# Optimization experiments

Measured on AMD Instinct MI355X. Metric: run time of the kernel, lower is better.

Reference implementation:

```python
import jax, jax.numpy as jnp
import numpy as np

K = 3       # conv-transpose kernel size
STRIDE = 2  # conv-transpose stride
PAD = 1     # conv-transpose padding
POOL = 6    # fused pool: MaxPool3d(2,2) then MaxPool3d(3,3) == MaxPool3d(6,6)


def setup_inputs() -> dict:
    key = jax.random.key(0)
    k1, k2, k3 = jax.random.split(key, 3)
    x = jax.random.normal(k1, (8, 16, 32, 32, 32), dtype=jnp.float32)
    weight = jax.random.normal(k2, (16, 32, K, K, K), dtype=jnp.float32)  # [C_in, C_out, k, k, k]
    bias = jax.random.normal(k3, (32,), dtype=jnp.float32)
    return {"x": x, "weight": weight, "bias": bias}


def _conv_transpose3d(x, weight, bias):
    # Transposed conv as dilated conv: lhs_dilation=stride, pad k-1-p, flip kernel.
    # weight layout [C_in, C_out, kd, kh, kw] matches kernel spec 'IODHW'.
    pad = K - 1 - PAD
    y = jax.lax.conv_general_dilated(
        x,
        jnp.flip(weight, axis=(2, 3, 4)),
        window_strides=(1, 1, 1),
        padding=[(pad, pad)] * 3,
        lhs_dilation=(STRIDE, STRIDE, STRIDE),
        dimension_numbers=("NCDHW", "IODHW", "NCDHW"),
    )
    return y + bias[None, :, None, None, None]


def reference(x, weight, bias):
    y = _conv_transpose3d(x, weight, bias)  # [N, C_out, 63, 63, 63]
    n, c, d, h, w = y.shape
    do, ho, wo = d // POOL, h // POOL, w // POOL
    # fused non-overlapping 6x6x6 max pool (== MaxPool3d(2) -> MaxPool3d(3))
    y = y[:, :, : do * POOL, : ho * POOL, : wo * POOL]
    y = y.reshape(n, c, do, POOL, ho, POOL, wo, POOL).max(axis=(3, 5, 7))
    # channel sum, keepdim -> [N, 1, do, ho, wo]
    return jnp.sum(y, axis=1, keepdims=True)
```

## Files before the change

### kernel.cpp

```cpp
#include <hip/hip_runtime.h>
#include <hip/hip_bf16.h>
#include <math.h>


namespace {

typedef __attribute__((ext_vector_type(8))) short short8;
typedef __attribute__((ext_vector_type(16))) float f32x16;

__constant__ int JK[27] = {13, 12, 14, 10, 16, 9,  11, 15, 17, 4,  22, 3,  5, 21,
                           23, 1,  7,  19, 25, 0,  2,  6,  8,  18, 20, 24, 26};

__device__ __forceinline__ uint f2bf(float f) {
  uint u = __float_as_uint(f);
  return (u + 0x7FFFu + ((u >> 16) & 1u)) >> 16;
}

__global__ void prep_w(const float* __restrict__ w, ushort* __restrict__ w2) {
  const int o = blockIdx.x * 256 + threadIdx.x;
  const int t2 = o >> 9;
  const int cih = (o >> 8) & 1;
  const int co = (o >> 3) & 31;
  const int ci = cih * 8 + (o & 7);
  w2[o] = (ushort)f2bf(w[(ci * 32 + co) * 27 + JK[t2]]);
}

template <int PA, int PB, int PC, int BASE>
__device__ __forceinline__ float cls_max(const ushort* __restrict__ w2l,
                                         const char* __restrict__ xw, int lin0,
                                         int lin1, int sz0, int sz1, int hi) {
  constexpr int NTZ = PA ? 2 : 1, NTY = PB ? 2 : 1, NTX = PC ? 2 : 1;
  constexpr int NT = NTZ * NTY * NTX;
  short8 bv[NT];
#pragma unroll
  for (int t = 0; t < NT; ++t)
    bv[t] = *reinterpret_cast<const short8*>(w2l + (BASE + t) * 512);

  f32x16 d;
#pragma unroll
  for (int i = 0; i < 16; ++i) d[i] = 0.f;
#pragma unroll
  for (int a = 0; a < NTZ; ++a) {
    const int oz = PA ? (a ? 0 : 1) : 0;
#pragma unroll
    for (int b = 0; b < NTY; ++b) {
      const int oy = PB ? (b ? 0 : 1) : 0;
#pragma unroll
      for (int c = 0; c < NTX; ++c) {
        const int ox = PC ? (c ? 0 : 1) : 0;
        const int addr =
            ((oz ? lin1 : lin0) + (oy * 4 + ox) * 48) ^ (oz ? sz1 : sz0);
        const short8 av = *reinterpret_cast<const short8*>(xw + addr);
        d = __builtin_amdgcn_mfma_f32_32x32x16_bf16(
            av, bv[(a * NTY + b) * NTX + c], d, 0, 0, 0);
      }
    }
  }
  float ma = d[0];
#pragma unroll
  for (int i = 1; i < 12; ++i) ma = fmaxf(ma, d[i]);
  const float mb = fmaxf(d[12], fmaxf(d[13], d[14]));
  return hi ? ma : fmaxf(ma, mb);
}

__global__ __launch_bounds__(256, 4) void fused_mfma(
    const float* __restrict__ x, const ushort* __restrict__ w2,
    const float* __restrict__ bias, float* __restrict__ out) {
  __shared__ __align__(16) char xls[4 * 3072];

  const int t = threadIdx.x;
  const int wv = t >> 6;
  const int l = t & 63;
  const int hi = l >> 5;
  const int co = l & 31;

  const int cell = blockIdx.x * 4 + wv;
  const int pw = cell % 10;
  const int ph = (cell / 10) % 10;
  const int pd = (cell / 100) % 10;
  const int n = cell / 1000;

  char* xw = xls + wv * 3072;
  {
    const int xi = l & 3, yi = (l >> 2) & 3, zi = l >> 4;
    const float* xg = x + (size_t)n * 524288 + (size_t)(3 * pd + zi) * 1024 +
                      (3 * ph + yi) * 32 + (3 * pw + xi);
    uint pk[8];
#pragma unroll
    for (int q = 0; q < 8; ++q) {
      const uint h0 = f2bf(xg[(2 * q) * 32768]);
      const uint h1 = f2bf(xg[(2 * q + 1) * 32768]);
      pk[q] = (h0 & 0xFFFFu) | (h1 << 16);
    }
    const int swz = (zi & 3) << 4;
    const int a0 = (l * 48) ^ swz;
    const int a1 = (l * 48 + 16) ^ swz;
    *reinterpret_cast<uint4*>(xw + a0) = make_uint4(pk[0], pk[1], pk[2], pk[3]);
    *reinterpret_cast<uint4*>(xw + a1) = make_uint4(pk[4], pk[5], pk[6], pk[7]);
  }
  asm volatile("s_waitcnt lgkmcnt(0)" ::: "memory");

  int p = co > 26 ? 26 : co;
  const int ip = p / 9, jp = (p / 3) % 3, kp = p % 3;
  const int lin0 = (ip * 16 + jp * 4 + kp) * 48 + hi * 16;
  const int lin1 = ((ip + 1) * 16 + jp * 4 + kp) * 48 + hi * 16;
  const int sz0 = (ip & 3) << 4;
  const int sz1 = ((ip + 1) & 3) << 4;

  const ushort* w2l = w2 + hi * 256 + co * 8;

  float cm = cls_max<1, 1, 1, 19>(w2l, xw, lin0, lin1, sz0, sz1, hi);
  cm = fmaxf(cm, cls_max<1, 1, 0, 15>(w2l, xw, lin0, lin1, sz0, sz1, hi));
  cm = fmaxf(cm, cls_max<1, 0, 1, 11>(w2l, xw, lin0, lin1, sz0, sz1, hi));
  cm = fmaxf(cm, cls_max<1, 0, 0, 9>(w2l, xw, lin0, lin1, sz0, sz1, hi));
  cm = fmaxf(cm, cls_max<0, 1, 1, 5>(w2l, xw, lin0, lin1, sz0, sz1, hi));
  cm = fmaxf(cm, cls_max<0, 1, 0, 3>(w2l, xw, lin0, lin1, sz0, sz1, hi));
  cm = fmaxf(cm, cls_max<0, 0, 1, 1>(w2l, xw, lin0, lin1, sz0, sz1, hi));
  cm = fmaxf(cm, cls_max<0, 0, 0, 0>(w2l, xw, lin0, lin1, sz0, sz1, hi));
  cm = fmaxf(cm, __shfl_xor(cm, 32));

  float r = cm + bias[co];
#pragma unroll
  for (int off = 16; off >= 1; off >>= 1) r += __shfl_xor(r, off);
  if (l == 0) out[cell] = r;
}

}

extern "C" void kernel_launch(void* const* d_in, const int* in_sizes, int n_in,
                              void* d_out, int out_size, void* d_ws,
                              size_t ws_size, hipStream_t stream) {
  const float* x = (const float*)d_in[0];
  const float* w = (const float*)d_in[1];
  const float* b = (const float*)d_in[2];
  float* out = (float*)d_out;
  ushort* w2 = (ushort*)d_ws;
  prep_w<<<54, 256, 0, stream>>>(w, w2);
  fused_mfma<<<2000, 256, 0, stream>>>(x, w2, b, out);
}
```

Baseline: 81.96 us.

## Load a whole pooled row per block with coalesced float4 loads and split classes

Each block now handles a full row of 10 pooled cells for one (n, pd, ph) instead of one cell per wave. The shared input slab is loaded cooperatively with float4 reads and written in a swizzled bf16 layout, which replaces the strided scalar gathers and removes the overlap between neighbouring cells. The eight parity classes are split into two halves assigned to different waves, and partial maxima are combined through shared memory after a block barrier. Blocks are also remapped across batch indices. The costs are a block-wide sync, extra shared memory for the reductions, and weights that are no longer preloaded into registers.

```diff
diff --git a/kernel.cpp b/kernel.cpp
--- a/kernel.cpp
+++ b/kernel.cpp
@@ -1,5 +1,4 @@
 #include <hip/hip_runtime.h>
-#include <hip/hip_bf16.h>
 #include <math.h>
 
 
@@ -25,20 +24,24 @@
   w2[o] = (ushort)f2bf(w[(ci * 32 + co) * 27 + JK[t2]]);
 }
 
-template <int PA, int PB, int PC, int BASE>
-__device__ __forceinline__ float cls_max(const ushort* __restrict__ w2l,
-                                         const char* __restrict__ xw, int lin0,
-                                         int lin1, int sz0, int sz1, int hi) {
+struct Pre {
+  uint a[2][2][2];
+};
+
+__device__ __forceinline__ f32x16 zero16() {
+  f32x16 d;
+#pragma unroll
+  for (int i = 0; i < 16; ++i) d[i] = 0.f;
+  return d;
+}
+
+template <int CC, int BASE>
+__device__ __forceinline__ void class_accum(f32x16& d,
+                                            const ushort* __restrict__ w2l,
+                                            const Pre& pre,
+                                            const char* __restrict__ xb) {
+  constexpr int PA = (CC >> 2) & 1, PB = (CC >> 1) & 1, PC = CC & 1;
   constexpr int NTZ = PA ? 2 : 1, NTY = PB ? 2 : 1, NTX = PC ? 2 : 1;
-  constexpr int NT = NTZ * NTY * NTX;
-  short8 bv[NT];
-#pragma unroll
-  for (int t = 0; t < NT; ++t)
-    bv[t] = *reinterpret_cast<const short8*>(w2l + (BASE + t) * 512);
-
-  f32x16 d;
-#pragma unroll
-  for (int i = 0; i < 16; ++i) d[i] = 0.f;
 #pragma unroll
   for (int a = 0; a < NTZ; ++a) {
     const int oz = PA ? (a ? 0 : 1) : 0;
@@ -48,25 +51,73 @@
 #pragma unroll
       for (int c = 0; c < NTX; ++c) {
         const int ox = PC ? (c ? 0 : 1) : 0;
-        const int addr =
-            ((oz ? lin1 : lin0) + (oy * 4 + ox) * 48) ^ (oz ? sz1 : sz0);
-        const short8 av = *reinterpret_cast<const short8*>(xw + addr);
-        d = __builtin_amdgcn_mfma_f32_32x32x16_bf16(
-            av, bv[(a * NTY + b) * NTX + c], d, 0, 0, 0);
+        const short8 bv = *reinterpret_cast<const short8*>(
+            w2l + (BASE + (a * NTY + b) * NTX + c) * 512);
+        const short8 av =
+            *reinterpret_cast<const short8*>(xb + pre.a[oz][oy][ox]);
+        d = __builtin_amdgcn_mfma_f32_32x32x16_bf16(av, bv, d, 0, 0, 0);
       }
     }
   }
+}
+
+__device__ __forceinline__ float rowmax(const f32x16& d, int hi) {
   float ma = d[0];
 #pragma unroll
   for (int i = 1; i < 12; ++i) ma = fmaxf(ma, d[i]);
-  const float mb = fmaxf(d[12], fmaxf(d[13], d[14]));
+  const float mb = fmaxf(fmaxf(d[12], d[13]), d[14]);
   return hi ? ma : fmaxf(ma, mb);
+}
+
+template <int SP>
+__device__ __forceinline__ void do_cell(int pw, int l, int hi, int co, int kp,
+                                        const uint lin[2][2],
+                                        const int zy4[2][2],
+                                        const ushort* __restrict__ w2l,
+                                        const ushort* __restrict__ xs,
+                                        float* __restrict__ red) {
+  Pre pre;
+  const int cellk = 3 * pw + kp;
+#pragma unroll
+  for (int oz = 0; oz < 2; ++oz)
+#pragma unroll
+    for (int oy = 0; oy < 2; ++oy)
+#pragma unroll
+      for (int ox = 0; ox < 2; ++ox) {
+        const int xcol = cellk + ox;
+        pre.a[oz][oy][ox] = (lin[oz][oy] + (uint)(xcol << 5)) ^
+                            ((uint)(((zy4[oz][oy] ^ (xcol >> 2)) & 7)) << 4);
+      }
+  const char* xb = reinterpret_cast<const char*>(xs);
+
+  f32x16 d = zero16();
+  if (SP == 0) class_accum<7, 19>(d, w2l, pre, xb);
+  else         class_accum<6, 15>(d, w2l, pre, xb);
+  float m = rowmax(d, hi);
+  d = zero16();
+  if (SP == 0) class_accum<0, 0>(d, w2l, pre, xb);
+  else         class_accum<1, 1>(d, w2l, pre, xb);
+  m = fmaxf(m, rowmax(d, hi));
+  m = fmaxf(m, __shfl_xor(m, 32));
+  if (l < 32) red[(pw * 4 + (SP == 0 ? 0 : 1)) * 32 + co] = m;
+
+  d = zero16();
+  if (SP == 0) class_accum<5, 11>(d, w2l, pre, xb);
+  else         class_accum<3, 5>(d, w2l, pre, xb);
+  m = rowmax(d, hi);
+  d = zero16();
+  if (SP == 0) class_accum<2, 3>(d, w2l, pre, xb);
+  else         class_accum<4, 9>(d, w2l, pre, xb);
+  m = fmaxf(m, rowmax(d, hi));
+  m = fmaxf(m, __shfl_xor(m, 32));
+  if (l < 32) red[(pw * 4 + (SP == 0 ? 2 : 3)) * 32 + co] = m;
 }
 
 __global__ __launch_bounds__(256, 4) void fused_mfma(
     const float* __restrict__ x, const ushort* __restrict__ w2,
     const float* __restrict__ bias, float* __restrict__ out) {
-  __shared__ __align__(16) char xls[4 * 3072];
+  __shared__ __align__(16) ushort xs[8192];
+  __shared__ float red[10 * 4 * 32];
 
   const int t = threadIdx.x;
   const int wv = t >> 6;
@@ -74,55 +125,67 @@
   const int hi = l >> 5;
   const int co = l & 31;
 
-  const int cell = blockIdx.x * 4 + wv;
-  const int pw = cell % 10;
-  const int ph = (cell / 10) % 10;
-  const int pd = (cell / 100) % 10;
-  const int n = cell / 1000;
-
-  char* xw = xls + wv * 3072;
+  const int lb = (blockIdx.x & 7) * 100 + (blockIdx.x >> 3);
+  const int n = lb / 100, pd = (lb / 10) % 10, ph = lb % 10;
+
   {
-    const int xi = l & 3, yi = (l >> 2) & 3, zi = l >> 4;
-    const float* xg = x + (size_t)n * 524288 + (size_t)(3 * pd + zi) * 1024 +
-                      (3 * ph + yi) * 32 + (3 * pw + xi);
-    uint pk[8];
-#pragma unroll
-    for (int q = 0; q < 8; ++q) {
-      const uint h0 = f2bf(xg[(2 * q) * 32768]);
-      const uint h1 = f2bf(xg[(2 * q + 1) * 32768]);
-      pk[q] = (h0 & 0xFFFFu) | (h1 << 16);
+    const float* xg =
+        x + (size_t)n * 524288 + (size_t)(3 * pd) * 1024 + (3 * ph) * 32;
+#pragma unroll
+    for (int j = 0; j < 8; ++j) {
+      const int fi = j * 256 + t;
+      const int r = fi >> 3;
+      const int xq = fi & 7;
+      const int ci = r >> 4, z = (r >> 2) & 3, y = r & 3;
+      const float4 v = *reinterpret_cast<const float4*>(
+          xg + (size_t)ci * 32768 + z * 1024 + y * 32 + xq * 4);
+      const uint base = (uint)((z << 12) + (y << 10) + ((ci >> 3) << 4) +
+                               ((ci & 7) << 1));
+      const uint swz = (uint)((((z * 4 + y) ^ xq) & 7)) << 4;
+      char* xb = reinterpret_cast<char*>(xs);
+      *(ushort*)(xb + ((base + ((uint)(4 * xq + 0) << 5)) ^ swz)) =
+          (ushort)f2bf(v.x);
+      *(ushort*)(xb + ((base + ((uint)(4 * xq + 1) << 5)) ^ swz)) =
+          (ushort)f2bf(v.y);
+      *(ushort*)(xb + ((base + ((uint)(4 * xq + 2) << 5)) ^ swz)) =
+          (ushort)f2bf(v.z);
+      *(ushort*)(xb + ((base + ((uint)(4 * xq + 3) << 5)) ^ swz)) =
+          (ushort)f2bf(v.w);
     }
-    const int swz = (zi & 3) << 4;
-    const int a0 = (l * 48) ^ swz;
-    const int a1 = (l * 48 + 16) ^ swz;
-    *reinterpret_cast<uint4*>(xw + a0) = make_uint4(pk[0], pk[1], pk[2], pk[3]);
-    *reinterpret_cast<uint4*>(xw + a1) = make_uint4(pk[4], pk[5], pk[6], pk[7]);
   }
-  asm volatile("s_waitcnt lgkmcnt(0)" ::: "memory");
-
-  int p = co > 26 ? 26 : co;
+  __syncthreads();
+
+  const int p = co > 26 ? 26 : co;
   const int ip = p / 9, jp = (p / 3) % 3, kp = p % 3;
-  const int lin0 = (ip * 16 + jp * 4 + kp) * 48 + hi * 16;
-  const int lin1 = ((ip + 1) * 16 + jp * 4 + kp) * 48 + hi * 16;
-  const int sz0 = (ip & 3) << 4;
-  const int sz1 = ((ip + 1) & 3) << 4;
+  uint lin[2][2];
+  int zy4[2][2];
+#pragma unroll
+  for (int oz = 0; oz < 2; ++oz)
+#pragma unroll
+    for (int oy = 0; oy < 2; ++oy) {
+      const int z = ip + oz, y = jp + oy;
+      lin[oz][oy] = (uint)((z << 12) + (y << 10) + (hi << 4));
+      zy4[oz][oy] = z * 4 + y;
+    }
 
   const ushort* w2l = w2 + hi * 256 + co * 8;
 
-  float cm = cls_max<1, 1, 1, 19>(w2l, xw, lin0, lin1, sz0, sz1, hi);
-  cm = fmaxf(cm, cls_max<1, 1, 0, 15>(w2l, xw, lin0, lin1, sz0, sz1, hi));
-  cm = fmaxf(cm, cls_max<1, 0, 1, 11>(w2l, xw, lin0, lin1, sz0, sz1, hi));
-  cm = fmaxf(cm, cls_max<1, 0, 0, 9>(w2l, xw, lin0, lin1, sz0, sz1, hi));
-  cm = fmaxf(cm, cls_max<0, 1, 1, 5>(w2l, xw, lin0, lin1, sz0, sz1, hi));
-  cm = fmaxf(cm, cls_max<0, 1, 0, 3>(w2l, xw, lin0, lin1, sz0, sz1, hi));
-  cm = fmaxf(cm, cls_max<0, 0, 1, 1>(w2l, xw, lin0, lin1, sz0, sz1, hi));
-  cm = fmaxf(cm, cls_max<0, 0, 0, 0>(w2l, xw, lin0, lin1, sz0, sz1, hi));
-  cm = fmaxf(cm, __shfl_xor(cm, 32));
-
-  float r = cm + bias[co];
-#pragma unroll
-  for (int off = 16; off >= 1; off >>= 1) r += __shfl_xor(r, off);
-  if (l == 0) out[cell] = r;
+  for (int c = wv; c < 10; c += 4)
+    do_cell<0>(c, l, hi, co, kp, lin, zy4, w2l, xs, red);
+  for (int c = (wv + 2) & 3; c < 10; c += 4)
+    do_cell<1>(c, l, hi, co, kp, lin, zy4, w2l, xs, red);
+
+  __syncthreads();
+
+  for (int c = wv; c < 10; c += 4) {
+    float v = red[(c * 4 + 0) * 32 + co];
+#pragma unroll
+    for (int s = 1; s < 4; ++s) v = fmaxf(v, red[(c * 4 + s) * 32 + co]);
+    v += bias[co];
+#pragma unroll
+    for (int off = 16; off >= 1; off >>= 1) v += __shfl_xor(v, off);
+    if (l == 0) out[lb * 10 + c] = v;
+  }
 }
 
 }
@@ -136,5 +199,5 @@
   float* out = (float*)d_out;
   ushort* w2 = (ushort*)d_ws;
   prep_w<<<54, 256, 0, stream>>>(w, w2);
-  fused_mfma<<<2000, 256, 0, stream>>>(x, w2, b, out);
-}
+  fused_mfma<<<800, 256, 0, stream>>>(x, w2, b, out);
+}
```

New measurement: 80.33 us. -2.0%, faster.
